# Kernel tuning notes

Hardware: AMD Instinct MI355X
Metric: run time of the kernel (lower is better)

Reference implementation:

```python
import jax, jax.numpy as jnp
import numpy as np

NUM_LEVELS = 16
LEVEL_DIM = 2
BASE_RES = 32
PER_LEVEL_SCALE = 2.0
TABLE_SIZE = 2 ** 19  # padded size of every level's table
RES = np.array([int(BASE_RES * PER_LEVEL_SCALE ** i) for i in range(NUM_LEVELS)], dtype=np.float32)
SIZES = np.minimum(RES.astype(np.float64) ** 3, TABLE_SIZE).astype(np.float32)  # true table sizes
NEAR, FAR, NUM_SAMPLES = 0.1, 1.5, 64
N_RAYS = 16384


def _xavier(key, fin, fout):
    lim = float(np.sqrt(6.0 / (fin + fout)))
    return jax.random.uniform(key, (fin, fout), jnp.float32, -lim, lim)


def setup_inputs() -> dict:
    key = jax.random.key(0)
    ks = jax.random.split(key, 12)
    rays_o = jax.random.uniform(ks[0], (N_RAYS, 3), jnp.float32, -0.5, 0.5)
    d = jax.random.normal(ks[1], (N_RAYS, 3), jnp.float32)
    rays_d = d / jnp.linalg.norm(d, axis=-1, keepdims=True)
    tables = jax.random.uniform(ks[2], (NUM_LEVELS, TABLE_SIZE, LEVEL_DIM), jnp.float32, -1e-4, 1e-4)
    return {
        'rays_o': rays_o, 'rays_d': rays_d, 'tables': tables,
        'Wg0': _xavier(ks[3], 32, 64), 'bg0': jnp.zeros((64,), jnp.float32),
        'Wg1': _xavier(ks[4], 64, 64), 'bg1': jnp.zeros((64,), jnp.float32),
        'Wd': _xavier(ks[5], 64, 16), 'bd': jnp.zeros((16,), jnp.float32),
        'Wc0': _xavier(ks[6], 24, 64), 'bc0': jnp.zeros((64,), jnp.float32),
        'Wc1': _xavier(ks[7], 64, 64), 'bc1': jnp.zeros((64,), jnp.float32),
        'Wc2': _xavier(ks[8], 64, 64), 'bc2': jnp.zeros((64,), jnp.float32),
        'Wch': _xavier(ks[9], 64, 3), 'bch': jnp.zeros((3,), jnp.float32),
    }


def _hash_encode(pts, tables):
    # pts: [N, S, 3] in roughly [-1, 1]; tables: [L, T, 2]
    res = jnp.asarray(RES)            # [L]
    sizes = jnp.asarray(SIZES)        # [L]
    scaled = (pts[..., None, :] + 1.0) / 2.0 * (res[:, None] - 1.0)     # [N,S,L,3]
    scaled = jnp.clip(scaled, 0.0, res[:, None] - 1.0)
    # torch computes the flat index in float then .long() (truncation), then clamps to table size
    idx_f = scaled[..., 0] * res * res + scaled[..., 1] * res + scaled[..., 2]  # [N,S,L]
    idx = jnp.minimum(idx_f, sizes - 1.0).astype(jnp.int32)
    feats = tables[jnp.arange(NUM_LEVELS)[None, None, :], idx]          # [N,S,L,2]
    return feats.reshape(feats.shape[:-2] + (NUM_LEVELS * LEVEL_DIM,))  # [N,S,32]


def _sh_encode(d):
    # degree-4 encoder in the source only ever builds 9 features
    x, y, z = d[..., 0], d[..., 1], d[..., 2]
    return jnp.stack([jnp.full_like(x, 0.5), x, y, z,
                      x * y, x * z, y * z, x * x - y * y, 3.0 * z * z - 1.0], axis=-1)  # [N,9]


def reference(rays_o, rays_d, tables, Wg0, bg0, Wg1, bg1, Wd, bd,
              Wc0, bc0, Wc1, bc1, Wc2, bc2, Wch, bch):
    n = rays_o.shape[0]
    # --- stratified-free (eval mode) sampling along rays ---
    t = jnp.linspace(0.0, 1.0, NUM_SAMPLES, dtype=jnp.float32)
    z_vals = jnp.broadcast_to(NEAR + (FAR - NEAR) * t, (n, NUM_SAMPLES))           # [N,S]
    pts = rays_o[:, None, :] + rays_d[:, None, :] * z_vals[..., None]              # [N,S,3]
    # --- LoDAwareNeRF forward ---
    feats = _hash_encode(pts, tables)                                              # [N,S,32]
    h = jax.nn.relu(feats @ Wg0 + bg0)
    h = jax.nn.relu(h @ Wg1 + bg1)
    geo = h @ Wd + bd                                                              # [N,S,16]
    density = jax.nn.softplus(geo[..., 0] - 1.0)                                   # [N,S]
    geo_feat = geo[..., 1:]                                                        # [N,S,15]
    dir_f = jnp.broadcast_to(_sh_encode(rays_d)[:, None, :], (n, NUM_SAMPLES, 9))  # [N,S,9]
    c = jnp.concatenate([geo_feat, dir_f], axis=-1)                                # [N,S,24]
    c = jax.nn.relu(c @ Wc0 + bc0)
    c = jax.nn.relu(c @ Wc1 + bc1)
    c = jax.nn.relu(c @ Wc2 + bc2)
    color = jax.nn.sigmoid(c @ Wch + bch)                                          # [N,S,3]
    # --- volume rendering compositing ---
    dists = z_vals[..., 1:] - z_vals[..., :-1]
    dists = jnp.concatenate([dists, jnp.full_like(dists[..., :1], 1e10)], axis=-1)
    dists = dists * jnp.linalg.norm(rays_d, axis=-1, keepdims=True)
    alpha = 1.0 - jnp.exp(-density * dists)                                        # [N,S]
    T = jnp.cumprod(1.0 - alpha + 1e-10, axis=-1)
    T = jnp.concatenate([jnp.ones_like(T[..., :1]), T[..., :-1]], axis=-1)
    weights = alpha * T                                                            # [N,S]
    rgb = jnp.sum(weights[..., None] * color, axis=-2)                             # [N,3]
    depth = jnp.sum(weights * z_vals, axis=-1)                                     # [N]
    acc = jnp.sum(weights, axis=-1)                                                # [N]
    return rgb, depth, acc, weights
```

## Files before the change

### kernel.cpp

```cpp
#include <hip/hip_runtime.h>
#include <hip/hip_bf16.h>
#include <math.h>

typedef float  f32x4 __attribute__((ext_vector_type(4)));
typedef short  s16x8 __attribute__((ext_vector_type(8)));
typedef unsigned int u32x2 __attribute__((ext_vector_type(2)));
typedef unsigned int u32x4 __attribute__((ext_vector_type(4)));

constexpr int kNRays = 16384;
constexpr int kOffDepth   = kNRays * 3;
constexpr int kOffAcc     = kOffDepth + kNRays;
constexpr int kOffWeights = kOffAcc + kNRays;

constexpr int kWg0 = 0;
constexpr int kWg1 = 2048;
constexpr int kWd  = 6144;
constexpr int kWc0 = 7168;
constexpr int kWc1 = 9216;
constexpr int kWc2 = 13312;
constexpr int kWch = 17408;
constexpr int kWsTotal = 18432;

__device__ __forceinline__ ushort f2bf(float x) {
    unsigned u = __float_as_uint(x);
    return (ushort)((u + 0x7FFFu + ((u >> 16) & 1u)) >> 16);
}
__device__ __forceinline__ unsigned pk2(float lo, float hi) {
    __hip_bfloat162 h = __float22bfloat162_rn(float2{lo, hi});
    return *reinterpret_cast<unsigned*>(&h);
}
__device__ __forceinline__ float sel4(float v0, float v1, float v2, float v3, int s) {
    float a = (s & 1) ? v1 : v0;
    float b = (s & 1) ? v3 : v2;
    return (s & 2) ? b : a;
}
__device__ __forceinline__ float wave_sum(float v) {
#pragma unroll
    for (int off = 32; off > 0; off >>= 1) v += __shfl_xor(v, off, 64);
    return v;
}

__global__ __launch_bounds__(256) void prep_weights(
    const float* __restrict__ Wg0, const float* __restrict__ Wg1,
    const float* __restrict__ Wd,  const float* __restrict__ Wc0,
    const float* __restrict__ Wc1, const float* __restrict__ Wc2,
    const float* __restrict__ Wch, const float* __restrict__ bc0,
    ushort* __restrict__ ws)
{
    const int i = blockIdx.x * 256 + threadIdx.x;
    if (i >= kWsTotal) return;
    const float* W; int FIN, FOUT, KT, base; bool dperm = false, c0bias = false;
    if (i < kWg1)      { W = Wg0; FIN = 32; FOUT = 64; KT = 1; base = kWg0; }
    else if (i < kWd)  { W = Wg1; FIN = 64; FOUT = 64; KT = 2; base = kWg1; }
    else if (i < kWc0) { W = Wd;  FIN = 64; FOUT = 16; KT = 2; base = kWd; dperm = true; }
    else if (i < kWc1) { W = Wc0; FIN = 24; FOUT = 64; KT = 1; base = kWc0; c0bias = true; }
    else if (i < kWc2) { W = Wc1; FIN = 64; FOUT = 64; KT = 2; base = kWc1; }
    else if (i < kWch) { W = Wc2; FIN = 64; FOUT = 64; KT = 2; base = kWc2; }
    else               { W = Wch; FIN = 64; FOUT = 3;  KT = 2; base = kWch; }
    const int r = i - base;
    const int e = r & 7, l = (r >> 3) & 63, t = r >> 9;
    const int kt = t % KT, mt = t / KT;
    const int k = kt * 32 + ((l >> 4) << 3) + e;
    int j = mt * 16 + (l & 15);
    if (dperm) j = (j == 15) ? 0 : j + 1;
    float w = 0.0f;
    if (k < FIN && j < FOUT) w = W[k * FOUT + j];
    if (c0bias && k == 24 && j < FOUT) w = bc0[j];
    ws[i] = f2bf(w);
}

template<int KT, bool HASBIAS>
__device__ __forceinline__ void layer64(ushort* __restrict__ Xw,
                                        const ushort* __restrict__ Aws,
                                        const float* __restrict__ bias,
                                        const int* rp, const int* wa,
                                        int g, int lane) {
    s16x8 B[KT][4];
#pragma unroll
    for (int kt = 0; kt < KT; ++kt)
#pragma unroll
        for (int nt = 0; nt < 4; ++nt)
            B[kt][nt] = *(const s16x8*)&Xw[rp[kt * 4 + nt]];
#pragma unroll
    for (int mt = 0; mt < 4; ++mt) {
        const s16x8 A0 = *(const s16x8*)&Aws[((mt * KT + 0) * 64 + lane) * 8];
        s16x8 A1;
        if constexpr (KT == 2) A1 = *(const s16x8*)&Aws[((mt * KT + 1) * 64 + lane) * 8];
        f32x4 b;
        if constexpr (HASBIAS) b = *(const f32x4*)(bias + mt * 16 + g * 4);
        else                   b = (f32x4){ 0.f, 0.f, 0.f, 0.f };
        f32x4 acc[4];
#pragma unroll
        for (int nt = 0; nt < 4; ++nt) {
            acc[nt] = b;
            acc[nt] = __builtin_amdgcn_mfma_f32_16x16x32_bf16(A0, B[0][nt], acc[nt], 0, 0, 0);
            if constexpr (KT == 2)
                acc[nt] = __builtin_amdgcn_mfma_f32_16x16x32_bf16(A1, B[1][nt], acc[nt], 0, 0, 0);
        }
#pragma unroll
        for (int nt = 0; nt < 4; ++nt) {
            const float x0 = fmaxf(acc[nt].x, 0.f), x1 = fmaxf(acc[nt].y, 0.f);
            const float x2 = fmaxf(acc[nt].z, 0.f), x3 = fmaxf(acc[nt].w, 0.f);
            *(u32x2*)&Xw[wa[mt * 4 + nt]] = (u32x2){ pk2(x0, x1), pk2(x2, x3) };
        }
    }
}

__device__ __forceinline__ void layer16(const ushort* __restrict__ Xw,
                                        const ushort* __restrict__ Aws,
                                        const int* rp, int lane, f32x4 acc[4]) {
    const s16x8 A0 = *(const s16x8*)&Aws[(0 * 64 + lane) * 8];
    const s16x8 A1 = *(const s16x8*)&Aws[(1 * 64 + lane) * 8];
#pragma unroll
    for (int nt = 0; nt < 4; ++nt) {
        const s16x8 B0 = *(const s16x8*)&Xw[rp[0 * 4 + nt]];
        acc[nt] = __builtin_amdgcn_mfma_f32_16x16x32_bf16(A0, B0, acc[nt], 0, 0, 0);
        const s16x8 B1 = *(const s16x8*)&Xw[rp[1 * 4 + nt]];
        acc[nt] = __builtin_amdgcn_mfma_f32_16x16x32_bf16(A1, B1, acc[nt], 0, 0, 0);
    }
}

__global__ __launch_bounds__(256, 4) void nerf_mfma_kernel(
    const float* __restrict__ rays_o, const float* __restrict__ rays_d,
    const float* __restrict__ tables, const ushort* __restrict__ ws,
    const float* __restrict__ bg0, const float* __restrict__ bg1,
    const float* __restrict__ bd,  const float* __restrict__ bc1,
    const float* __restrict__ bc2, const float* __restrict__ bch,
    float* __restrict__ out)
{
    __shared__ __align__(16) ushort Xs[4 * 4096];
    const int tid  = threadIdx.x;
    const int wid  = tid >> 6;
    const int lane = tid & 63;
    const int c16  = lane & 15;
    const int g    = lane >> 4;
    const int ray  = blockIdx.x * 4 + wid;
    ushort* Xw = Xs + wid * 4096;

    const float ox = rays_o[ray * 3 + 0], oy = rays_o[ray * 3 + 1], oz = rays_o[ray * 3 + 2];
    const float dx = rays_d[ray * 3 + 0], dy = rays_d[ray * 3 + 1], dz = rays_d[ray * 3 + 2];

    const float step = 1.0f / 63.0f;
    const float z  = 0.1f + 1.4f * ((float)lane * step);
    const float zn = 0.1f + 1.4f * ((float)(lane + 1) * step);

    int rp[8], wa[16];
#pragma unroll
    for (int kt = 0; kt < 2; ++kt)
#pragma unroll
        for (int nt = 0; nt < 4; ++nt)
            rp[kt * 4 + nt] = (nt * 16 + c16) * 64 + 8 * ((kt * 4 + g) ^ (c16 & 7));
#pragma unroll
    for (int mt = 0; mt < 4; ++mt)
#pragma unroll
        for (int nt = 0; nt < 4; ++nt)
            wa[mt * 4 + nt] = (nt * 16 + c16) * 64
                            + 8 * ((2 * mt + (g >> 1)) ^ (c16 & 7)) + 4 * (g & 1);

    const float2* __restrict__ tb = (const float2*)tables;
    const float tc = (float)c16 * step;
    s16x8 B0f[4];
#pragma unroll
    for (int nt = 0; nt < 4; ++nt) {
        const float ts = tc + (float)nt * (16.0f / 63.0f);
        const float zs = fmaf(1.4f, ts, 0.1f);
        const float px = fmaf(dx, zs, ox), py = fmaf(dy, zs, oy), pz = fmaf(dz, zs, oz);
        u32x4 val;
#pragma unroll
        for (int j = 0; j < 4; ++j) {
            const int lv = g * 4 + j;
            const float res = (float)(32 << lv);
            const float rm1 = res - 1.0f;
            const float h = 0.5f * rm1;
            const float sx = __builtin_amdgcn_fmed3f(fmaf(px, h, h), 0.f, rm1);
            const float sy = __builtin_amdgcn_fmed3f(fmaf(py, h, h), 0.f, rm1);
            const float sz = __builtin_amdgcn_fmed3f(fmaf(pz, h, h), 0.f, rm1);
            const float idxf = fmaf(sx, res * res, fmaf(sy, res, sz));
            const float szm1 = (lv == 0) ? 32767.f : (lv == 1) ? 262143.f : 524287.f;
            const unsigned idx = (unsigned)(int)fminf(idxf, szm1);
            const float2 f2 = tb[((unsigned)lv << 19) + idx];
            val[j] = pk2(f2.x, f2.y);
        }
        B0f[nt] = *(const s16x8*)&val;
    }

#pragma unroll
    for (int mt = 0; mt < 4; ++mt) {
        const s16x8 A0 = *(const s16x8*)&ws[kWg0 + (mt * 64 + lane) * 8];
        const f32x4 b = *(const f32x4*)(bg0 + mt * 16 + g * 4);
        f32x4 acc[4];
#pragma unroll
        for (int nt = 0; nt < 4; ++nt) {
            acc[nt] = b;
            acc[nt] = __builtin_amdgcn_mfma_f32_16x16x32_bf16(A0, B0f[nt], acc[nt], 0, 0, 0);
        }
#pragma unroll
        for (int nt = 0; nt < 4; ++nt) {
            const float x0 = fmaxf(acc[nt].x, 0.f), x1 = fmaxf(acc[nt].y, 0.f);
            const float x2 = fmaxf(acc[nt].z, 0.f), x3 = fmaxf(acc[nt].w, 0.f);
            *(u32x2*)&Xw[wa[mt * 4 + nt]] = (u32x2){ pk2(x0, x1), pk2(x2, x3) };
        }
    }

    layer64<2, true>(Xw, ws + kWg1, bg1, rp, wa, g, lane);

    f32x4 accd[4];
    {
        const float db0 = bd[g * 4 + 1];
        const float db1 = bd[g * 4 + 2];
        const float db2 = bd[g * 4 + 3];
        const int i3 = (g == 3) ? 0 : g * 4 + 4;
        const float db3 = bd[i3];
        const f32x4 b = { db0, db1, db2, db3 };
#pragma unroll
        for (int nt = 0; nt < 4; ++nt) accd[nt] = b;
    }
    layer16(Xw, ws + kWd, rp, lane, accd);
    const float lgit = sel4(__shfl(accd[0].w, 48 + c16, 64),
                            __shfl(accd[1].w, 48 + c16, 64),
                            __shfl(accd[2].w, 48 + c16, 64),
                            __shfl(accd[3].w, 48 + c16, 64), g);
#pragma unroll
    for (int nt = 0; nt < 4; ++nt)
        *(u32x2*)&Xw[wa[nt]] = (u32x2){ pk2(accd[nt].x, accd[nt].y),
                                        pk2(accd[nt].z, accd[nt].w) };
    Xw[lane * 64 + 8 * (1 ^ (lane & 7)) + 7] = 0x3F00;
    {
        u32x4 w = { pk2(dx, dy), pk2(dz, dx * dy), pk2(dx * dz, dy * dz),
                    pk2(dx * dx - dy * dy, 3.f * dz * dz - 1.f) };
        *(u32x4*)&Xw[lane * 64 + 8 * (2 ^ (lane & 7))] = w;
    }
    {
        u32x4 w = { 0x00003F80u, 0u, 0u, 0u };
        *(u32x4*)&Xw[lane * 64 + 8 * (3 ^ (lane & 7))] = w;
    }

    layer64<1, false>(Xw, ws + kWc0, nullptr, rp, wa, g, lane);
    layer64<2, true >(Xw, ws + kWc1, bc1,     rp, wa, g, lane);
    layer64<2, true >(Xw, ws + kWc2, bc2,     rp, wa, g, lane);

    f32x4 accc[4];
    {
        const float cb0 = bch[0], cb1 = bch[1], cb2 = bch[2];
        const f32x4 b = (g == 0) ? (f32x4){ cb0, cb1, cb2, 0.f } : (f32x4){ 0.f, 0.f, 0.f, 0.f };
#pragma unroll
        for (int nt = 0; nt < 4; ++nt) accc[nt] = b;
    }
    layer16(Xw, ws + kWch, rp, lane, accc);
    const float lr = sel4(__shfl(accc[0].x, c16, 64), __shfl(accc[1].x, c16, 64),
                          __shfl(accc[2].x, c16, 64), __shfl(accc[3].x, c16, 64), g);
    const float lgr = sel4(__shfl(accc[0].y, c16, 64), __shfl(accc[1].y, c16, 64),
                           __shfl(accc[2].y, c16, 64), __shfl(accc[3].y, c16, 64), g);
    const float lb = sel4(__shfl(accc[0].z, c16, 64), __shfl(accc[1].z, c16, 64),
                          __shfl(accc[2].z, c16, 64), __shfl(accc[3].z, c16, 64), g);

    const float cr = 1.f / (1.f + expf(-lr));
    const float cg = 1.f / (1.f + expf(-lgr));
    const float cb = 1.f / (1.f + expf(-lb));
    const float gx = lgit - 1.0f;
    const float density = fmaxf(gx, 0.f) + log1pf(expf(-fabsf(gx)));

    const float dnorm = sqrtf(dx * dx + dy * dy + dz * dz);
    float dist = (lane < 63) ? (zn - z) : 1e10f;
    dist *= dnorm;
    const float alpha = 1.0f - expf(-density * dist);
    float f = 1.0f - alpha + 1e-10f;
#pragma unroll
    for (int off = 1; off < 64; off <<= 1) {
        const float gg = __shfl_up(f, off, 64);
        if (lane >= off) f *= gg;
    }
    float T = __shfl_up(f, 1, 64);
    if (lane == 0) T = 1.0f;
    const float w = alpha * T;

    out[kOffWeights + ray * 64 + lane] = w;
    const float sr = wave_sum(w * cr);
    const float sg = wave_sum(w * cg);
    const float sb = wave_sum(w * cb);
    const float sd = wave_sum(w * z);
    const float sa = wave_sum(w);
    if (lane == 0) {
        out[ray * 3 + 0] = sr;
        out[ray * 3 + 1] = sg;
        out[ray * 3 + 2] = sb;
        out[kOffDepth + ray] = sd;
        out[kOffAcc + ray]   = sa;
    }
}

extern "C" void kernel_launch(void* const* d_in, const int* in_sizes, int n_in,
                              void* d_out, int out_size, void* d_ws, size_t ws_size,
                              hipStream_t stream) {
    const float* rays_o = (const float*)d_in[0];
    const float* rays_d = (const float*)d_in[1];
    const float* tables = (const float*)d_in[2];
    const float* Wg0 = (const float*)d_in[3];
    const float* bg0 = (const float*)d_in[4];
    const float* Wg1 = (const float*)d_in[5];
    const float* bg1 = (const float*)d_in[6];
    const float* Wd  = (const float*)d_in[7];
    const float* bd  = (const float*)d_in[8];
    const float* Wc0 = (const float*)d_in[9];
    const float* bc0 = (const float*)d_in[10];
    const float* Wc1 = (const float*)d_in[11];
    const float* bc1 = (const float*)d_in[12];
    const float* Wc2 = (const float*)d_in[13];
    const float* bc2 = (const float*)d_in[14];
    const float* Wch = (const float*)d_in[15];
    const float* bch = (const float*)d_in[16];
    float* out = (float*)d_out;
    ushort* wsp = (ushort*)d_ws;

    prep_weights<<<dim3((kWsTotal + 255) / 256), dim3(256), 0, stream>>>(
        Wg0, Wg1, Wd, Wc0, Wc1, Wc2, Wch, bc0, wsp);

    nerf_mfma_kernel<<<dim3(kNRays / 4), dim3(256), 0, stream>>>(
        rays_o, rays_d, tables, wsp,
        bg0, bg1, bd, bc1, bc2, bch, out);
}
```

Measured before the change: 78.86 us.

## Keep MLP activations in registers using 32x32 MFMA and permlane32 swaps

Replaces the 16x16x32 MFMA layers that round-trip activations through LDS with 32x32x16 MFMA layers whose outputs are rearranged into the next layer's B operand via permlane32_swap, removing shared memory entirely. The weight prep kernel is changed to the new A-fragment layout and also stages the density and color-head biases. This is meant to remove LDS writes and reads and the swizzle address math between layers. In exchange it raises register pressure, and launch bounds drop to 3 waves per block-occupancy hint.

```diff
diff --git a/kernel.cpp b/kernel.cpp
--- a/kernel.cpp
+++ b/kernel.cpp
@@ -2,9 +2,9 @@
 #include <hip/hip_bf16.h>
 #include <math.h>
 
-typedef float  f32x4 __attribute__((ext_vector_type(4)));
-typedef short  s16x8 __attribute__((ext_vector_type(8)));
-typedef unsigned int u32x2 __attribute__((ext_vector_type(2)));
+typedef float  f32x4  __attribute__((ext_vector_type(4)));
+typedef float  f32x16 __attribute__((ext_vector_type(16)));
+typedef short  s16x8  __attribute__((ext_vector_type(8)));
 typedef unsigned int u32x4 __attribute__((ext_vector_type(4)));
 
 constexpr int kNRays = 16384;
@@ -12,27 +12,23 @@
 constexpr int kOffAcc     = kOffDepth + kNRays;
 constexpr int kOffWeights = kOffAcc + kNRays;
 
-constexpr int kWg0 = 0;
-constexpr int kWg1 = 2048;
-constexpr int kWd  = 6144;
-constexpr int kWc0 = 7168;
-constexpr int kWc1 = 9216;
-constexpr int kWc2 = 13312;
-constexpr int kWch = 17408;
-constexpr int kWsTotal = 18432;
+constexpr int kAg0 = 0;
+constexpr int kAg1 = 2048;
+constexpr int kAd  = 6144;
+constexpr int kAc0 = 8192;
+constexpr int kAc1 = 10240;
+constexpr int kAc2 = 14336;
+constexpr int kAch = 18432;
+constexpr int kFb  = 20480;
+constexpr int kPrepTotal = 20480 + 64;
 
 __device__ __forceinline__ ushort f2bf(float x) {
     unsigned u = __float_as_uint(x);
     return (ushort)((u + 0x7FFFu + ((u >> 16) & 1u)) >> 16);
 }
 __device__ __forceinline__ unsigned pk2(float lo, float hi) {
-    __hip_bfloat162 h = __float22bfloat162_rn(float2{lo, hi});
-    return *reinterpret_cast<unsigned*>(&h);
-}
-__device__ __forceinline__ float sel4(float v0, float v1, float v2, float v3, int s) {
-    float a = (s & 1) ? v1 : v0;
-    float b = (s & 1) ? v3 : v2;
-    return (s & 2) ? b : a;
+    __hip_bfloat162 hh = __float22bfloat162_rn(float2{lo, hi});
+    return *reinterpret_cast<unsigned*>(&hh);
 }
 __device__ __forceinline__ float wave_sum(float v) {
 #pragma unroll
@@ -45,97 +41,103 @@
     const float* __restrict__ Wd,  const float* __restrict__ Wc0,
     const float* __restrict__ Wc1, const float* __restrict__ Wc2,
     const float* __restrict__ Wch, const float* __restrict__ bc0,
+    const float* __restrict__ bd,  const float* __restrict__ bch,
     ushort* __restrict__ ws)
 {
     const int i = blockIdx.x * 256 + threadIdx.x;
-    if (i >= kWsTotal) return;
-    const float* W; int FIN, FOUT, KT, base; bool dperm = false, c0bias = false;
-    if (i < kWg1)      { W = Wg0; FIN = 32; FOUT = 64; KT = 1; base = kWg0; }
-    else if (i < kWd)  { W = Wg1; FIN = 64; FOUT = 64; KT = 2; base = kWg1; }
-    else if (i < kWc0) { W = Wd;  FIN = 64; FOUT = 16; KT = 2; base = kWd; dperm = true; }
-    else if (i < kWc1) { W = Wc0; FIN = 24; FOUT = 64; KT = 1; base = kWc0; c0bias = true; }
-    else if (i < kWc2) { W = Wc1; FIN = 64; FOUT = 64; KT = 2; base = kWc1; }
-    else if (i < kWch) { W = Wc2; FIN = 64; FOUT = 64; KT = 2; base = kWc2; }
-    else               { W = Wch; FIN = 64; FOUT = 3;  KT = 2; base = kWch; }
-    const int r = i - base;
-    const int e = r & 7, l = (r >> 3) & 63, t = r >> 9;
-    const int kt = t % KT, mt = t / KT;
-    const int k = kt * 32 + ((l >> 4) << 3) + e;
-    int j = mt * 16 + (l & 15);
-    if (dperm) j = (j == 15) ? 0 : j + 1;
-    float w = 0.0f;
-    if (k < FIN && j < FOUT) w = W[k * FOUT + j];
-    if (c0bias && k == 24 && j < FOUT) w = bc0[j];
-    ws[i] = f2bf(w);
-}
-
-template<int KT, bool HASBIAS>
-__device__ __forceinline__ void layer64(ushort* __restrict__ Xw,
+    if (i >= kPrepTotal) return;
+    if (i < kFb) {
+        const float* W; int KS, base, mode = 0;
+        if (i < kAg1)      { W = Wg0; KS = 2; base = kAg0; }
+        else if (i < kAd)  { W = Wg1; KS = 4; base = kAg1; }
+        else if (i < kAc0) { W = Wd;  KS = 4; base = kAd;  mode = 1; }
+        else if (i < kAc1) { W = Wc0; KS = 2; base = kAc0; mode = 2; }
+        else if (i < kAc2) { W = Wc1; KS = 4; base = kAc1; }
+        else if (i < kAch) { W = Wc2; KS = 4; base = kAc2; }
+        else               { W = Wch; KS = 4; base = kAch; mode = 3; }
+        const int r = i - base;
+        const int e = r & 7, l = (r >> 3) & 63, f = r >> 9;
+        const int ks = f % KS, mt = f / KS;
+        const int m = mt * 32 + (l & 31);
+        const int k = ks * 16 + (l >> 5) * 8 + e;
+        float w = 0.f;
+        if (mode == 0)      w = W[k * 64 + m];
+        else if (mode == 1) w = (m < 15) ? W[k * 16 + m + 1] : (m == 15 ? W[k * 16] : 0.f);
+        else if (mode == 2) w = (k < 24) ? W[k * 64 + m] : (k == 24 ? bc0[m] : 0.f);
+        else                w = (m < 3) ? W[k * 3 + m] : 0.f;
+        ws[i] = f2bf(w);
+    } else {
+        float* fb = (float*)(ws + kFb);
+        const int t = i - kFb;
+        float v = 0.f;
+        if (t < 32) { if (t < 15) v = bd[t + 1]; else if (t == 15) v = bd[0]; }
+        else        { const int tt = t - 32; if (tt < 3) v = bch[tt]; }
+        fb[t] = v;
+    }
+}
+
+template<int KS, bool HASBIAS>
+__device__ __forceinline__ void layer32(const u32x4 (*__restrict__ Bi)[2],
                                         const ushort* __restrict__ Aws,
                                         const float* __restrict__ bias,
-                                        const int* rp, const int* wa,
-                                        int g, int lane) {
-    s16x8 B[KT][4];
-#pragma unroll
-    for (int kt = 0; kt < KT; ++kt)
-#pragma unroll
-        for (int nt = 0; nt < 4; ++nt)
-            B[kt][nt] = *(const s16x8*)&Xw[rp[kt * 4 + nt]];
-#pragma unroll
-    for (int mt = 0; mt < 4; ++mt) {
-        const s16x8 A0 = *(const s16x8*)&Aws[((mt * KT + 0) * 64 + lane) * 8];
-        s16x8 A1;
-        if constexpr (KT == 2) A1 = *(const s16x8*)&Aws[((mt * KT + 1) * 64 + lane) * 8];
-        f32x4 b;
-        if constexpr (HASBIAS) b = *(const f32x4*)(bias + mt * 16 + g * 4);
-        else                   b = (f32x4){ 0.f, 0.f, 0.f, 0.f };
-        f32x4 acc[4];
-#pragma unroll
-        for (int nt = 0; nt < 4; ++nt) {
-            acc[nt] = b;
-            acc[nt] = __builtin_amdgcn_mfma_f32_16x16x32_bf16(A0, B[0][nt], acc[nt], 0, 0, 0);
-            if constexpr (KT == 2)
-                acc[nt] = __builtin_amdgcn_mfma_f32_16x16x32_bf16(A1, B[1][nt], acc[nt], 0, 0, 0);
-        }
-#pragma unroll
-        for (int nt = 0; nt < 4; ++nt) {
-            const float x0 = fmaxf(acc[nt].x, 0.f), x1 = fmaxf(acc[nt].y, 0.f);
-            const float x2 = fmaxf(acc[nt].z, 0.f), x3 = fmaxf(acc[nt].w, 0.f);
-            *(u32x2*)&Xw[wa[mt * 4 + nt]] = (u32x2){ pk2(x0, x1), pk2(x2, x3) };
-        }
-    }
-}
-
-__device__ __forceinline__ void layer16(const ushort* __restrict__ Xw,
-                                        const ushort* __restrict__ Aws,
-                                        const int* rp, int lane, f32x4 acc[4]) {
-    const s16x8 A0 = *(const s16x8*)&Aws[(0 * 64 + lane) * 8];
-    const s16x8 A1 = *(const s16x8*)&Aws[(1 * 64 + lane) * 8];
-#pragma unroll
-    for (int nt = 0; nt < 4; ++nt) {
-        const s16x8 B0 = *(const s16x8*)&Xw[rp[0 * 4 + nt]];
-        acc[nt] = __builtin_amdgcn_mfma_f32_16x16x32_bf16(A0, B0, acc[nt], 0, 0, 0);
-        const s16x8 B1 = *(const s16x8*)&Xw[rp[1 * 4 + nt]];
-        acc[nt] = __builtin_amdgcn_mfma_f32_16x16x32_bf16(A1, B1, acc[nt], 0, 0, 0);
-    }
-}
-
-__global__ __launch_bounds__(256, 4) void nerf_mfma_kernel(
+                                        int h, int lane,
+                                        u32x4 (*__restrict__ Bo)[2]) {
+#pragma unroll
+    for (int mt = 0; mt < 2; ++mt) {
+        s16x8 A[KS];
+#pragma unroll
+        for (int ks = 0; ks < KS; ++ks)
+            A[ks] = *(const s16x8*)&Aws[((mt * KS + ks) * 64 + lane) * 8];
+        f32x4 bq[4];
+#pragma unroll
+        for (int r8 = 0; r8 < 4; ++r8) {
+            if constexpr (HASBIAS)
+                bq[r8] = *(const f32x4*)(bias + mt * 32 + 4 * h + 8 * r8);
+            else
+                bq[r8] = (f32x4){0.f, 0.f, 0.f, 0.f};
+        }
+#pragma unroll
+        for (int nt = 0; nt < 2; ++nt) {
+            f32x16 acc;
+#pragma unroll
+            for (int r8 = 0; r8 < 4; ++r8) {
+                acc[4 * r8 + 0] = bq[r8].x; acc[4 * r8 + 1] = bq[r8].y;
+                acc[4 * r8 + 2] = bq[r8].z; acc[4 * r8 + 3] = bq[r8].w;
+            }
+#pragma unroll
+            for (int ks = 0; ks < KS; ++ks)
+                acc = __builtin_amdgcn_mfma_f32_32x32x16_bf16(
+                    A[ks], *(const s16x8*)&Bi[ks][nt], acc, 0, 0, 0);
+            unsigned q[4][2];
+#pragma unroll
+            for (int r8 = 0; r8 < 4; ++r8)
+#pragma unroll
+                for (int t = 0; t < 2; ++t)
+                    q[r8][t] = pk2(fmaxf(acc[4 * r8 + 2 * t], 0.f),
+                                   fmaxf(acc[4 * r8 + 2 * t + 1], 0.f));
+#pragma unroll
+            for (int kk = 0; kk < 2; ++kk) {
+                auto s0 = __builtin_amdgcn_permlane32_swap(q[2 * kk][0], q[2 * kk + 1][0], false, false);
+                auto s1 = __builtin_amdgcn_permlane32_swap(q[2 * kk][1], q[2 * kk + 1][1], false, false);
+                Bo[2 * mt + kk][nt] = (u32x4){ s0[0], s1[0], s0[1], s1[1] };
+            }
+        }
+    }
+}
+
+__global__ __launch_bounds__(256, 3) void nerf_mfma_kernel(
     const float* __restrict__ rays_o, const float* __restrict__ rays_d,
     const float* __restrict__ tables, const ushort* __restrict__ ws,
     const float* __restrict__ bg0, const float* __restrict__ bg1,
-    const float* __restrict__ bd,  const float* __restrict__ bc1,
-    const float* __restrict__ bc2, const float* __restrict__ bch,
+    const float* __restrict__ bc1, const float* __restrict__ bc2,
     float* __restrict__ out)
 {
-    __shared__ __align__(16) ushort Xs[4 * 4096];
     const int tid  = threadIdx.x;
     const int wid  = tid >> 6;
     const int lane = tid & 63;
-    const int c16  = lane & 15;
-    const int g    = lane >> 4;
+    const int c    = lane & 31;
+    const int h    = lane >> 5;
     const int ray  = blockIdx.x * 4 + wid;
-    ushort* Xw = Xs + wid * 4096;
 
     const float ox = rays_o[ray * 3 + 0], oy = rays_o[ray * 3 + 1], oz = rays_o[ray * 3 + 2];
     const float dx = rays_d[ray * 3 + 0], dy = rays_d[ray * 3 + 1], dz = rays_d[ray * 3 + 2];
@@ -144,115 +146,116 @@
     const float z  = 0.1f + 1.4f * ((float)lane * step);
     const float zn = 0.1f + 1.4f * ((float)(lane + 1) * step);
 
-    int rp[8], wa[16];
-#pragma unroll
-    for (int kt = 0; kt < 2; ++kt)
-#pragma unroll
-        for (int nt = 0; nt < 4; ++nt)
-            rp[kt * 4 + nt] = (nt * 16 + c16) * 64 + 8 * ((kt * 4 + g) ^ (c16 & 7));
-#pragma unroll
-    for (int mt = 0; mt < 4; ++mt)
-#pragma unroll
-        for (int nt = 0; nt < 4; ++nt)
-            wa[mt * 4 + nt] = (nt * 16 + c16) * 64
-                            + 8 * ((2 * mt + (g >> 1)) ^ (c16 & 7)) + 4 * (g & 1);
-
     const float2* __restrict__ tb = (const float2*)tables;
-    const float tc = (float)c16 * step;
-    s16x8 B0f[4];
-#pragma unroll
-    for (int nt = 0; nt < 4; ++nt) {
-        const float ts = tc + (float)nt * (16.0f / 63.0f);
+    u32x4 B0[2][2];
+#pragma unroll
+    for (int nt = 0; nt < 2; ++nt) {
+        const int s = nt * 32 + c;
+        const float ts = (float)s * step;
         const float zs = fmaf(1.4f, ts, 0.1f);
         const float px = fmaf(dx, zs, ox), py = fmaf(dy, zs, oy), pz = fmaf(dz, zs, oz);
-        u32x4 val;
-#pragma unroll
-        for (int j = 0; j < 4; ++j) {
-            const int lv = g * 4 + j;
-            const float res = (float)(32 << lv);
-            const float rm1 = res - 1.0f;
-            const float h = 0.5f * rm1;
-            const float sx = __builtin_amdgcn_fmed3f(fmaf(px, h, h), 0.f, rm1);
-            const float sy = __builtin_amdgcn_fmed3f(fmaf(py, h, h), 0.f, rm1);
-            const float sz = __builtin_amdgcn_fmed3f(fmaf(pz, h, h), 0.f, rm1);
-            const float idxf = fmaf(sx, res * res, fmaf(sy, res, sz));
-            const float szm1 = (lv == 0) ? 32767.f : (lv == 1) ? 262143.f : 524287.f;
-            const unsigned idx = (unsigned)(int)fminf(idxf, szm1);
-            const float2 f2 = tb[((unsigned)lv << 19) + idx];
-            val[j] = pk2(f2.x, f2.y);
-        }
-        B0f[nt] = *(const s16x8*)&val;
-    }
-
-#pragma unroll
-    for (int mt = 0; mt < 4; ++mt) {
-        const s16x8 A0 = *(const s16x8*)&ws[kWg0 + (mt * 64 + lane) * 8];
-        const f32x4 b = *(const f32x4*)(bg0 + mt * 16 + g * 4);
-        f32x4 acc[4];
-#pragma unroll
-        for (int nt = 0; nt < 4; ++nt) {
-            acc[nt] = b;
-            acc[nt] = __builtin_amdgcn_mfma_f32_16x16x32_bf16(A0, B0f[nt], acc[nt], 0, 0, 0);
-        }
-#pragma unroll
-        for (int nt = 0; nt < 4; ++nt) {
-            const float x0 = fmaxf(acc[nt].x, 0.f), x1 = fmaxf(acc[nt].y, 0.f);
-            const float x2 = fmaxf(acc[nt].z, 0.f), x3 = fmaxf(acc[nt].w, 0.f);
-            *(u32x2*)&Xw[wa[mt * 4 + nt]] = (u32x2){ pk2(x0, x1), pk2(x2, x3) };
-        }
-    }
-
-    layer64<2, true>(Xw, ws + kWg1, bg1, rp, wa, g, lane);
-
-    f32x4 accd[4];
+#pragma unroll
+        for (int ks = 0; ks < 2; ++ks) {
+            u32x4 val;
+#pragma unroll
+            for (int j = 0; j < 4; ++j) {
+                const int lv = 8 * ks + 4 * h + j;
+                const float res = (float)(32 << lv);
+                const float rm1 = res - 1.0f;
+                const float hf = 0.5f * rm1;
+                const float sx = __builtin_amdgcn_fmed3f(fmaf(px, hf, hf), 0.f, rm1);
+                const float sy = __builtin_amdgcn_fmed3f(fmaf(py, hf, hf), 0.f, rm1);
+                const float sz = __builtin_amdgcn_fmed3f(fmaf(pz, hf, hf), 0.f, rm1);
+                const float idxf = fmaf(sx, res * res, fmaf(sy, res, sz));
+                const float szm1 = (lv == 0) ? 32767.f : (lv == 1) ? 262143.f : 524287.f;
+                const unsigned idx = (unsigned)(int)fminf(idxf, szm1);
+                const float2 f2 = tb[((unsigned)lv << 19) + idx];
+                val[j] = pk2(f2.x, f2.y);
+            }
+            B0[ks][nt] = val;
+        }
+    }
+
+    u32x4 B1[4][2], B2[4][2];
+    layer32<2, true>(B0, ws + kAg0, bg0, h, lane, B1);
+    layer32<4, true>(B1, ws + kAg1, bg1, h, lane, B2);
+
+    const float* fb = (const float*)(ws + kFb);
+    u32x4 Bc0[2][2];
+    float lg0 = 0.f, lg1 = 0.f;
     {
-        const float db0 = bd[g * 4 + 1];
-        const float db1 = bd[g * 4 + 2];
-        const float db2 = bd[g * 4 + 3];
-        const int i3 = (g == 3) ? 0 : g * 4 + 4;
-        const float db3 = bd[i3];
-        const f32x4 b = { db0, db1, db2, db3 };
-#pragma unroll
-        for (int nt = 0; nt < 4; ++nt) accd[nt] = b;
-    }
-    layer16(Xw, ws + kWd, rp, lane, accd);
-    const float lgit = sel4(__shfl(accd[0].w, 48 + c16, 64),
-                            __shfl(accd[1].w, 48 + c16, 64),
-                            __shfl(accd[2].w, 48 + c16, 64),
-                            __shfl(accd[3].w, 48 + c16, 64), g);
-#pragma unroll
-    for (int nt = 0; nt < 4; ++nt)
-        *(u32x2*)&Xw[wa[nt]] = (u32x2){ pk2(accd[nt].x, accd[nt].y),
-                                        pk2(accd[nt].z, accd[nt].w) };
-    Xw[lane * 64 + 8 * (1 ^ (lane & 7)) + 7] = 0x3F00;
+        s16x8 Ad[4];
+#pragma unroll
+        for (int ks = 0; ks < 4; ++ks)
+            Ad[ks] = *(const s16x8*)&ws[kAd + (ks * 64 + lane) * 8];
+#pragma unroll
+        for (int nt = 0; nt < 2; ++nt) {
+            f32x16 acc;
+#pragma unroll
+            for (int r8 = 0; r8 < 4; ++r8) {
+                const f32x4 bq = *(const f32x4*)(fb + 4 * h + 8 * r8);
+                acc[4 * r8 + 0] = bq.x; acc[4 * r8 + 1] = bq.y;
+                acc[4 * r8 + 2] = bq.z; acc[4 * r8 + 3] = bq.w;
+            }
+#pragma unroll
+            for (int ks = 0; ks < 4; ++ks)
+                acc = __builtin_amdgcn_mfma_f32_32x32x16_bf16(
+                    Ad[ks], *(const s16x8*)&B2[ks][nt], acc, 0, 0, 0);
+            if (nt == 0) lg0 = acc[7]; else lg1 = acc[7];
+            if (h) acc[7] = 0.5f;
+            const unsigned q00 = pk2(acc[0], acc[1]), q01 = pk2(acc[2], acc[3]);
+            const unsigned q10 = pk2(acc[4], acc[5]), q11 = pk2(acc[6], acc[7]);
+            auto s0 = __builtin_amdgcn_permlane32_swap(q00, q10, false, false);
+            auto s1 = __builtin_amdgcn_permlane32_swap(q01, q11, false, false);
+            Bc0[0][nt] = (u32x4){ s0[0], s1[0], s0[1], s1[1] };
+        }
+    }
+    float lgit;
     {
-        u32x4 w = { pk2(dx, dy), pk2(dz, dx * dy), pk2(dx * dz, dy * dz),
-                    pk2(dx * dx - dy * dy, 3.f * dz * dz - 1.f) };
-        *(u32x4*)&Xw[lane * 64 + 8 * (2 ^ (lane & 7))] = w;
+        auto sl = __builtin_amdgcn_permlane32_swap(__float_as_uint(lg0), __float_as_uint(lg1), false, false);
+        lgit = __uint_as_float(sl[1]);
     }
     {
-        u32x4 w = { 0x00003F80u, 0u, 0u, 0u };
-        *(u32x4*)&Xw[lane * 64 + 8 * (3 ^ (lane & 7))] = w;
-    }
-
-    layer64<1, false>(Xw, ws + kWc0, nullptr, rp, wa, g, lane);
-    layer64<2, true >(Xw, ws + kWc1, bc1,     rp, wa, g, lane);
-    layer64<2, true >(Xw, ws + kWc2, bc2,     rp, wa, g, lane);
-
-    f32x4 accc[4];
+        u32x4 wloc;
+        if (h == 0) wloc = (u32x4){ pk2(dx, dy), pk2(dz, dx * dy), pk2(dx * dz, dy * dz),
+                                    pk2(dx * dx - dy * dy, 3.f * dz * dz - 1.f) };
+        else        wloc = (u32x4){ 0x00003F80u, 0u, 0u, 0u };
+        Bc0[1][0] = wloc; Bc0[1][1] = wloc;
+    }
+
+    u32x4 B3[4][2], B4[4][2], B5[4][2];
+    layer32<2, false>(Bc0, ws + kAc0, nullptr, h, lane, B3);
+    layer32<4, true >(B3,  ws + kAc1, bc1,     h, lane, B4);
+    layer32<4, true >(B4,  ws + kAc2, bc2,     h, lane, B5);
+
+    f32x16 acch[2];
     {
-        const float cb0 = bch[0], cb1 = bch[1], cb2 = bch[2];
-        const f32x4 b = (g == 0) ? (f32x4){ cb0, cb1, cb2, 0.f } : (f32x4){ 0.f, 0.f, 0.f, 0.f };
-#pragma unroll
-        for (int nt = 0; nt < 4; ++nt) accc[nt] = b;
-    }
-    layer16(Xw, ws + kWch, rp, lane, accc);
-    const float lr = sel4(__shfl(accc[0].x, c16, 64), __shfl(accc[1].x, c16, 64),
-                          __shfl(accc[2].x, c16, 64), __shfl(accc[3].x, c16, 64), g);
-    const float lgr = sel4(__shfl(accc[0].y, c16, 64), __shfl(accc[1].y, c16, 64),
-                           __shfl(accc[2].y, c16, 64), __shfl(accc[3].y, c16, 64), g);
-    const float lb = sel4(__shfl(accc[0].z, c16, 64), __shfl(accc[1].z, c16, 64),
-                          __shfl(accc[2].z, c16, 64), __shfl(accc[3].z, c16, 64), g);
+        s16x8 Ah[4];
+#pragma unroll
+        for (int ks = 0; ks < 4; ++ks)
+            Ah[ks] = *(const s16x8*)&ws[kAch + (ks * 64 + lane) * 8];
+#pragma unroll
+        for (int nt = 0; nt < 2; ++nt) {
+            f32x16 acc;
+#pragma unroll
+            for (int r8 = 0; r8 < 4; ++r8) {
+                const f32x4 bq = *(const f32x4*)(fb + 32 + 4 * h + 8 * r8);
+                acc[4 * r8 + 0] = bq.x; acc[4 * r8 + 1] = bq.y;
+                acc[4 * r8 + 2] = bq.z; acc[4 * r8 + 3] = bq.w;
+            }
+#pragma unroll
+            for (int ks = 0; ks < 4; ++ks)
+                acc = __builtin_amdgcn_mfma_f32_32x32x16_bf16(
+                    Ah[ks], *(const s16x8*)&B5[ks][nt], acc, 0, 0, 0);
+            acch[nt] = acc;
+        }
+    }
+    auto sw0 = __builtin_amdgcn_permlane32_swap(__float_as_uint(acch[0][0]), __float_as_uint(acch[1][0]), false, false);
+    auto sw1 = __builtin_amdgcn_permlane32_swap(__float_as_uint(acch[0][1]), __float_as_uint(acch[1][1]), false, false);
+    auto sw2 = __builtin_amdgcn_permlane32_swap(__float_as_uint(acch[0][2]), __float_as_uint(acch[1][2]), false, false);
+    const float lr  = __uint_as_float(sw0[0]);
+    const float lgr = __uint_as_float(sw1[0]);
+    const float lb  = __uint_as_float(sw2[0]);
 
     const float cr = 1.f / (1.f + expf(-lr));
     const float cg = 1.f / (1.f + expf(-lgr));
@@ -312,10 +315,10 @@
     float* out = (float*)d_out;
     ushort* wsp = (ushort*)d_ws;
 
-    prep_weights<<<dim3((kWsTotal + 255) / 256), dim3(256), 0, stream>>>(
-        Wg0, Wg1, Wd, Wc0, Wc1, Wc2, Wch, bc0, wsp);
+    prep_weights<<<dim3((kPrepTotal + 255) / 256), dim3(256), 0, stream>>>(
+        Wg0, Wg1, Wd, Wc0, Wc1, Wc2, Wch, bc0, bd, bch, wsp);
 
     nerf_mfma_kernel<<<dim3(kNRays / 4), dim3(256), 0, stream>>>(
         rays_o, rays_d, tables, wsp,
-        bg0, bg1, bd, bc1, bc2, bch, out);
-}
+        bg0, bg1, bc1, bc2, out);
+}
```

Result: slower. 85.39 us (+8.3%).

## Keep MLP activations in registers by permuting weight K-order, drop LDS staging

Applied to the files above, without the earlier changes.

Rewrites the MLP chain so each layer's MFMA output fragment is packed directly into the next layer's B operand in registers. The prep kernel permutes the weights' input-feature order so that the C layout lines up with B. This removes the shared-memory round trip, swizzled address tables and LDS stores/loads between layers. Biases for the density and color heads are prepacked into the workspace. Launch bounds drop from 4 to 3 blocks per SM, trading occupancy for the higher register pressure.

```diff
diff --git a/kernel.cpp b/kernel.cpp
--- a/kernel.cpp
+++ b/kernel.cpp
@@ -2,9 +2,8 @@
 #include <hip/hip_bf16.h>
 #include <math.h>
 
-typedef float  f32x4 __attribute__((ext_vector_type(4)));
-typedef short  s16x8 __attribute__((ext_vector_type(8)));
-typedef unsigned int u32x2 __attribute__((ext_vector_type(2)));
+typedef float  f32x4  __attribute__((ext_vector_type(4)));
+typedef short  s16x8  __attribute__((ext_vector_type(8)));
 typedef unsigned int u32x4 __attribute__((ext_vector_type(4)));
 
 constexpr int kNRays = 16384;
@@ -12,22 +11,23 @@
 constexpr int kOffAcc     = kOffDepth + kNRays;
 constexpr int kOffWeights = kOffAcc + kNRays;
 
-constexpr int kWg0 = 0;
-constexpr int kWg1 = 2048;
-constexpr int kWd  = 6144;
-constexpr int kWc0 = 7168;
-constexpr int kWc1 = 9216;
-constexpr int kWc2 = 13312;
-constexpr int kWch = 17408;
-constexpr int kWsTotal = 18432;
+constexpr int kAg0 = 0;
+constexpr int kAg1 = 2048;
+constexpr int kAd  = 6144;
+constexpr int kAc0 = 7168;
+constexpr int kAc1 = 9216;
+constexpr int kAc2 = 13312;
+constexpr int kAch = 17408;
+constexpr int kAF  = 18432;
+constexpr int kPrepTotal = kAF + 32;
 
 __device__ __forceinline__ ushort f2bf(float x) {
     unsigned u = __float_as_uint(x);
     return (ushort)((u + 0x7FFFu + ((u >> 16) & 1u)) >> 16);
 }
 __device__ __forceinline__ unsigned pk2(float lo, float hi) {
-    __hip_bfloat162 h = __float22bfloat162_rn(float2{lo, hi});
-    return *reinterpret_cast<unsigned*>(&h);
+    __hip_bfloat162 hh = __float22bfloat162_rn(float2{lo, hi});
+    return *reinterpret_cast<unsigned*>(&hh);
 }
 __device__ __forceinline__ float sel4(float v0, float v1, float v2, float v3, int s) {
     float a = (s & 1) ? v1 : v0;
@@ -44,98 +44,85 @@
     const float* __restrict__ Wg0, const float* __restrict__ Wg1,
     const float* __restrict__ Wd,  const float* __restrict__ Wc0,
     const float* __restrict__ Wc1, const float* __restrict__ Wc2,
-    const float* __restrict__ Wch, const float* __restrict__ bc0,
-    ushort* __restrict__ ws)
+    const float* __restrict__ Wch, const float* __restrict__ bd,
+    const float* __restrict__ bch, ushort* __restrict__ ws)
 {
     const int i = blockIdx.x * 256 + threadIdx.x;
-    if (i >= kWsTotal) return;
-    const float* W; int FIN, FOUT, KT, base; bool dperm = false, c0bias = false;
-    if (i < kWg1)      { W = Wg0; FIN = 32; FOUT = 64; KT = 1; base = kWg0; }
-    else if (i < kWd)  { W = Wg1; FIN = 64; FOUT = 64; KT = 2; base = kWg1; }
-    else if (i < kWc0) { W = Wd;  FIN = 64; FOUT = 16; KT = 2; base = kWd; dperm = true; }
-    else if (i < kWc1) { W = Wc0; FIN = 24; FOUT = 64; KT = 1; base = kWc0; c0bias = true; }
-    else if (i < kWc2) { W = Wc1; FIN = 64; FOUT = 64; KT = 2; base = kWc1; }
-    else if (i < kWch) { W = Wc2; FIN = 64; FOUT = 64; KT = 2; base = kWc2; }
-    else               { W = Wch; FIN = 64; FOUT = 3;  KT = 2; base = kWch; }
+    if (i >= kPrepTotal) return;
+    if (i >= kAF) {
+        float* fb = (float*)(ws + kAF);
+        const int t = i - kAF;
+        float v = 0.f;
+        if (t < 16) v = (t < 15) ? bd[t + 1] : bd[0];
+        else { const int tt = t - 16; if (tt < 3) v = bch[tt]; }
+        fb[t] = v;
+        return;
+    }
+    const float* W; int KTP, base, mode = 0;
+    if (i < kAg1)      { W = Wg0; KTP = 1; base = kAg0; }
+    else if (i < kAd)  { W = Wg1; KTP = 2; base = kAg1; }
+    else if (i < kAc0) { W = Wd;  KTP = 2; base = kAd;  mode = 1; }
+    else if (i < kAc1) { W = Wc0; KTP = 1; base = kAc0; mode = 2; }
+    else if (i < kAc2) { W = Wc1; KTP = 2; base = kAc1; }
+    else if (i < kAch) { W = Wc2; KTP = 2; base = kAc2; }
+    else               { W = Wch; KTP = 2; base = kAch; mode = 3; }
     const int r = i - base;
-    const int e = r & 7, l = (r >> 3) & 63, t = r >> 9;
-    const int kt = t % KT, mt = t / KT;
-    const int k = kt * 32 + ((l >> 4) << 3) + e;
-    int j = mt * 16 + (l & 15);
-    if (dperm) j = (j == 15) ? 0 : j + 1;
-    float w = 0.0f;
-    if (k < FIN && j < FOUT) w = W[k * FOUT + j];
-    if (c0bias && k == 24 && j < FOUT) w = bc0[j];
+    const int e = r & 7, l = (r >> 3) & 63, f = r >> 9;
+    const int kt = f % KTP, mt = f / KTP;
+    const int g = (l >> 4) & 3, c = l & 15;
+    const int fr = 32 * kt + ((e < 4) ? (4 * g + e) : (16 + 4 * g + (e - 4)));
+    const int m = 16 * mt + c;
+    float w = 0.f;
+    if (mode == 0)      w = W[fr * 64 + m];
+    else if (mode == 1) w = (m < 15) ? W[fr * 16 + m + 1] : W[fr * 16];
+    else if (mode == 2) w = (fr < 24) ? W[fr * 64 + m] : 0.f;
+    else                w = (m < 3) ? W[fr * 3 + m] : 0.f;
     ws[i] = f2bf(w);
 }
 
-template<int KT, bool HASBIAS>
-__device__ __forceinline__ void layer64(ushort* __restrict__ Xw,
-                                        const ushort* __restrict__ Aws,
-                                        const float* __restrict__ bias,
-                                        const int* rp, const int* wa,
-                                        int g, int lane) {
-    s16x8 B[KT][4];
-#pragma unroll
-    for (int kt = 0; kt < KT; ++kt)
-#pragma unroll
-        for (int nt = 0; nt < 4; ++nt)
-            B[kt][nt] = *(const s16x8*)&Xw[rp[kt * 4 + nt]];
+template<int KTP, bool RELU>
+__device__ __forceinline__ void layerX(const u32x4 (*__restrict__ Bi)[4],
+                                       const ushort* __restrict__ Aws,
+                                       const float* __restrict__ bias,
+                                       int g4, int lane, u32x4 (*__restrict__ Bo)[4]) {
 #pragma unroll
     for (int mt = 0; mt < 4; ++mt) {
-        const s16x8 A0 = *(const s16x8*)&Aws[((mt * KT + 0) * 64 + lane) * 8];
+        const s16x8 A0 = *(const s16x8*)&Aws[((mt * KTP + 0) * 64 + lane) * 8];
         s16x8 A1;
-        if constexpr (KT == 2) A1 = *(const s16x8*)&Aws[((mt * KT + 1) * 64 + lane) * 8];
-        f32x4 b;
-        if constexpr (HASBIAS) b = *(const f32x4*)(bias + mt * 16 + g * 4);
-        else                   b = (f32x4){ 0.f, 0.f, 0.f, 0.f };
-        f32x4 acc[4];
+        if constexpr (KTP == 2) A1 = *(const s16x8*)&Aws[((mt * KTP + 1) * 64 + lane) * 8];
+        const f32x4 C = *(const f32x4*)(bias + 16 * mt + g4);
 #pragma unroll
         for (int nt = 0; nt < 4; ++nt) {
-            acc[nt] = b;
-            acc[nt] = __builtin_amdgcn_mfma_f32_16x16x32_bf16(A0, B[0][nt], acc[nt], 0, 0, 0);
-            if constexpr (KT == 2)
-                acc[nt] = __builtin_amdgcn_mfma_f32_16x16x32_bf16(A1, B[1][nt], acc[nt], 0, 0, 0);
-        }
-#pragma unroll
-        for (int nt = 0; nt < 4; ++nt) {
-            const float x0 = fmaxf(acc[nt].x, 0.f), x1 = fmaxf(acc[nt].y, 0.f);
-            const float x2 = fmaxf(acc[nt].z, 0.f), x3 = fmaxf(acc[nt].w, 0.f);
-            *(u32x2*)&Xw[wa[mt * 4 + nt]] = (u32x2){ pk2(x0, x1), pk2(x2, x3) };
-        }
-    }
-}
-
-__device__ __forceinline__ void layer16(const ushort* __restrict__ Xw,
-                                        const ushort* __restrict__ Aws,
-                                        const int* rp, int lane, f32x4 acc[4]) {
-    const s16x8 A0 = *(const s16x8*)&Aws[(0 * 64 + lane) * 8];
-    const s16x8 A1 = *(const s16x8*)&Aws[(1 * 64 + lane) * 8];
-#pragma unroll
-    for (int nt = 0; nt < 4; ++nt) {
-        const s16x8 B0 = *(const s16x8*)&Xw[rp[0 * 4 + nt]];
-        acc[nt] = __builtin_amdgcn_mfma_f32_16x16x32_bf16(A0, B0, acc[nt], 0, 0, 0);
-        const s16x8 B1 = *(const s16x8*)&Xw[rp[1 * 4 + nt]];
-        acc[nt] = __builtin_amdgcn_mfma_f32_16x16x32_bf16(A1, B1, acc[nt], 0, 0, 0);
-    }
-}
-
-__global__ __launch_bounds__(256, 4) void nerf_mfma_kernel(
+            f32x4 acc = __builtin_amdgcn_mfma_f32_16x16x32_bf16(
+                A0, __builtin_bit_cast(s16x8, Bi[0][nt]), C, 0, 0, 0);
+            if constexpr (KTP == 2)
+                acc = __builtin_amdgcn_mfma_f32_16x16x32_bf16(
+                    A1, __builtin_bit_cast(s16x8, Bi[1][nt]), acc, 0, 0, 0);
+            float x0 = acc.x, x1 = acc.y, x2 = acc.z, x3 = acc.w;
+            if constexpr (RELU) {
+                x0 = fmaxf(x0, 0.f); x1 = fmaxf(x1, 0.f);
+                x2 = fmaxf(x2, 0.f); x3 = fmaxf(x3, 0.f);
+            }
+            Bo[mt >> 1][nt][2 * (mt & 1)]     = pk2(x0, x1);
+            Bo[mt >> 1][nt][2 * (mt & 1) + 1] = pk2(x2, x3);
+        }
+    }
+}
+
+__global__ __launch_bounds__(256, 3) void nerf_mfma_kernel(
     const float* __restrict__ rays_o, const float* __restrict__ rays_d,
     const float* __restrict__ tables, const ushort* __restrict__ ws,
     const float* __restrict__ bg0, const float* __restrict__ bg1,
-    const float* __restrict__ bd,  const float* __restrict__ bc1,
-    const float* __restrict__ bc2, const float* __restrict__ bch,
-    float* __restrict__ out)
+    const float* __restrict__ bc0, const float* __restrict__ bc1,
+    const float* __restrict__ bc2, float* __restrict__ out)
 {
-    __shared__ __align__(16) ushort Xs[4 * 4096];
     const int tid  = threadIdx.x;
     const int wid  = tid >> 6;
     const int lane = tid & 63;
     const int c16  = lane & 15;
     const int g    = lane >> 4;
+    const int g4   = 4 * g;
     const int ray  = blockIdx.x * 4 + wid;
-    ushort* Xw = Xs + wid * 4096;
 
     const float ox = rays_o[ray * 3 + 0], oy = rays_o[ray * 3 + 1], oz = rays_o[ray * 3 + 2];
     const float dx = rays_d[ray * 3 + 0], dy = rays_d[ray * 3 + 1], dz = rays_d[ray * 3 + 2];
@@ -144,115 +131,96 @@
     const float z  = 0.1f + 1.4f * ((float)lane * step);
     const float zn = 0.1f + 1.4f * ((float)(lane + 1) * step);
 
-    int rp[8], wa[16];
-#pragma unroll
-    for (int kt = 0; kt < 2; ++kt)
-#pragma unroll
-        for (int nt = 0; nt < 4; ++nt)
-            rp[kt * 4 + nt] = (nt * 16 + c16) * 64 + 8 * ((kt * 4 + g) ^ (c16 & 7));
-#pragma unroll
-    for (int mt = 0; mt < 4; ++mt)
-#pragma unroll
-        for (int nt = 0; nt < 4; ++nt)
-            wa[mt * 4 + nt] = (nt * 16 + c16) * 64
-                            + 8 * ((2 * mt + (g >> 1)) ^ (c16 & 7)) + 4 * (g & 1);
-
     const float2* __restrict__ tb = (const float2*)tables;
-    const float tc = (float)c16 * step;
-    s16x8 B0f[4];
+    u32x4 B0[1][4];
 #pragma unroll
     for (int nt = 0; nt < 4; ++nt) {
-        const float ts = tc + (float)nt * (16.0f / 63.0f);
+        const int s = nt * 16 + c16;
+        const float ts = (float)s * step;
         const float zs = fmaf(1.4f, ts, 0.1f);
         const float px = fmaf(dx, zs, ox), py = fmaf(dy, zs, oy), pz = fmaf(dz, zs, oz);
         u32x4 val;
 #pragma unroll
         for (int j = 0; j < 4; ++j) {
-            const int lv = g * 4 + j;
+            const int lv = (j < 2) ? (2 * g + j) : (8 + 2 * g + (j - 2));
             const float res = (float)(32 << lv);
             const float rm1 = res - 1.0f;
-            const float h = 0.5f * rm1;
-            const float sx = __builtin_amdgcn_fmed3f(fmaf(px, h, h), 0.f, rm1);
-            const float sy = __builtin_amdgcn_fmed3f(fmaf(py, h, h), 0.f, rm1);
-            const float sz = __builtin_amdgcn_fmed3f(fmaf(pz, h, h), 0.f, rm1);
+            const float hf = 0.5f * rm1;
+            const float sx = __builtin_amdgcn_fmed3f(fmaf(px, hf, hf), 0.f, rm1);
+            const float sy = __builtin_amdgcn_fmed3f(fmaf(py, hf, hf), 0.f, rm1);
+            const float sz = __builtin_amdgcn_fmed3f(fmaf(pz, hf, hf), 0.f, rm1);
             const float idxf = fmaf(sx, res * res, fmaf(sy, res, sz));
             const float szm1 = (lv == 0) ? 32767.f : (lv == 1) ? 262143.f : 524287.f;
             const unsigned idx = (unsigned)(int)fminf(idxf, szm1);
             const float2 f2 = tb[((unsigned)lv << 19) + idx];
             val[j] = pk2(f2.x, f2.y);
         }
-        B0f[nt] = *(const s16x8*)&val;
-    }
-
-#pragma unroll
-    for (int mt = 0; mt < 4; ++mt) {
-        const s16x8 A0 = *(const s16x8*)&ws[kWg0 + (mt * 64 + lane) * 8];
-        const f32x4 b = *(const f32x4*)(bg0 + mt * 16 + g * 4);
-        f32x4 acc[4];
-#pragma unroll
-        for (int nt = 0; nt < 4; ++nt) {
-            acc[nt] = b;
-            acc[nt] = __builtin_amdgcn_mfma_f32_16x16x32_bf16(A0, B0f[nt], acc[nt], 0, 0, 0);
-        }
-#pragma unroll
-        for (int nt = 0; nt < 4; ++nt) {
-            const float x0 = fmaxf(acc[nt].x, 0.f), x1 = fmaxf(acc[nt].y, 0.f);
-            const float x2 = fmaxf(acc[nt].z, 0.f), x3 = fmaxf(acc[nt].w, 0.f);
-            *(u32x2*)&Xw[wa[mt * 4 + nt]] = (u32x2){ pk2(x0, x1), pk2(x2, x3) };
-        }
-    }
-
-    layer64<2, true>(Xw, ws + kWg1, bg1, rp, wa, g, lane);
-
+        B0[0][nt] = val;
+    }
+
+    u32x4 B1[2][4], B2[2][4];
+    layerX<1, true>(B0, ws + kAg0, bg0, g4, lane, B1);
+    layerX<2, true>(B1, ws + kAg1, bg1, g4, lane, B2);
+
+    const float* fb = (const float*)(ws + kAF);
     f32x4 accd[4];
     {
-        const float db0 = bd[g * 4 + 1];
-        const float db1 = bd[g * 4 + 2];
-        const float db2 = bd[g * 4 + 3];
-        const int i3 = (g == 3) ? 0 : g * 4 + 4;
-        const float db3 = bd[i3];
-        const f32x4 b = { db0, db1, db2, db3 };
-#pragma unroll
-        for (int nt = 0; nt < 4; ++nt) accd[nt] = b;
-    }
-    layer16(Xw, ws + kWd, rp, lane, accd);
+        const s16x8 A0 = *(const s16x8*)&ws[kAd + (0 * 64 + lane) * 8];
+        const s16x8 A1 = *(const s16x8*)&ws[kAd + (1 * 64 + lane) * 8];
+        const f32x4 Cd = *(const f32x4*)(fb + g4);
+#pragma unroll
+        for (int nt = 0; nt < 4; ++nt) {
+            f32x4 a = __builtin_amdgcn_mfma_f32_16x16x32_bf16(
+                A0, __builtin_bit_cast(s16x8, B2[0][nt]), Cd, 0, 0, 0);
+            a = __builtin_amdgcn_mfma_f32_16x16x32_bf16(
+                A1, __builtin_bit_cast(s16x8, B2[1][nt]), a, 0, 0, 0);
+            accd[nt] = a;
+        }
+    }
     const float lgit = sel4(__shfl(accd[0].w, 48 + c16, 64),
                             __shfl(accd[1].w, 48 + c16, 64),
                             __shfl(accd[2].w, 48 + c16, 64),
                             __shfl(accd[3].w, 48 + c16, 64), g);
-#pragma unroll
-    for (int nt = 0; nt < 4; ++nt)
-        *(u32x2*)&Xw[wa[nt]] = (u32x2){ pk2(accd[nt].x, accd[nt].y),
-                                        pk2(accd[nt].z, accd[nt].w) };
-    Xw[lane * 64 + 8 * (1 ^ (lane & 7)) + 7] = 0x3F00;
+    const float dxy = dx * dy, dxz = dx * dz, dyz = dy * dz;
+    const float dqq = dx * dx - dy * dy, dzz = 3.f * dz * dz - 1.f;
+    const unsigned sh0 = pk2(sel4(dx, dxz, 0.f, 0.f, g), sel4(dy, dyz, 0.f, 0.f, g));
+    const unsigned sh1 = pk2(sel4(dz, dqq, 0.f, 0.f, g), sel4(dxy, dzz, 0.f, 0.f, g));
+    u32x4 Bc0[1][4];
+#pragma unroll
+    for (int nt = 0; nt < 4; ++nt) {
+        const f32x4 a = accd[nt];
+        const float a3 = (g == 3) ? 0.5f : a.w;
+        Bc0[0][nt][0] = pk2(a.x, a.y);
+        Bc0[0][nt][1] = pk2(a.z, a3);
+        Bc0[0][nt][2] = sh0;
+        Bc0[0][nt][3] = sh1;
+    }
+
+    u32x4 B3[2][4], B4[2][4], B5[2][4];
+    layerX<1, true>(Bc0, ws + kAc0, bc0, g4, lane, B3);
+    layerX<2, true>(B3,  ws + kAc1, bc1, g4, lane, B4);
+    layerX<2, true>(B4,  ws + kAc2, bc2, g4, lane, B5);
+
+    f32x4 acch[4];
     {
-        u32x4 w = { pk2(dx, dy), pk2(dz, dx * dy), pk2(dx * dz, dy * dz),
-                    pk2(dx * dx - dy * dy, 3.f * dz * dz - 1.f) };
-        *(u32x4*)&Xw[lane * 64 + 8 * (2 ^ (lane & 7))] = w;
-    }
-    {
-        u32x4 w = { 0x00003F80u, 0u, 0u, 0u };
-        *(u32x4*)&Xw[lane * 64 + 8 * (3 ^ (lane & 7))] = w;
-    }
-
-    layer64<1, false>(Xw, ws + kWc0, nullptr, rp, wa, g, lane);
-    layer64<2, true >(Xw, ws + kWc1, bc1,     rp, wa, g, lane);
-    layer64<2, true >(Xw, ws + kWc2, bc2,     rp, wa, g, lane);
-
-    f32x4 accc[4];
-    {
-        const float cb0 = bch[0], cb1 = bch[1], cb2 = bch[2];
-        const f32x4 b = (g == 0) ? (f32x4){ cb0, cb1, cb2, 0.f } : (f32x4){ 0.f, 0.f, 0.f, 0.f };
-#pragma unroll
-        for (int nt = 0; nt < 4; ++nt) accc[nt] = b;
-    }
-    layer16(Xw, ws + kWch, rp, lane, accc);
-    const float lr = sel4(__shfl(accc[0].x, c16, 64), __shfl(accc[1].x, c16, 64),
-                          __shfl(accc[2].x, c16, 64), __shfl(accc[3].x, c16, 64), g);
-    const float lgr = sel4(__shfl(accc[0].y, c16, 64), __shfl(accc[1].y, c16, 64),
-                           __shfl(accc[2].y, c16, 64), __shfl(accc[3].y, c16, 64), g);
-    const float lb = sel4(__shfl(accc[0].z, c16, 64), __shfl(accc[1].z, c16, 64),
-                          __shfl(accc[2].z, c16, 64), __shfl(accc[3].z, c16, 64), g);
+        const s16x8 A0 = *(const s16x8*)&ws[kAch + (0 * 64 + lane) * 8];
+        const s16x8 A1 = *(const s16x8*)&ws[kAch + (1 * 64 + lane) * 8];
+        const f32x4 Cc = *(const f32x4*)(fb + 16 + g4);
+#pragma unroll
+        for (int nt = 0; nt < 4; ++nt) {
+            f32x4 a = __builtin_amdgcn_mfma_f32_16x16x32_bf16(
+                A0, __builtin_bit_cast(s16x8, B5[0][nt]), Cc, 0, 0, 0);
+            a = __builtin_amdgcn_mfma_f32_16x16x32_bf16(
+                A1, __builtin_bit_cast(s16x8, B5[1][nt]), a, 0, 0, 0);
+            acch[nt] = a;
+        }
+    }
+    const float lr  = sel4(__shfl(acch[0].x, c16, 64), __shfl(acch[1].x, c16, 64),
+                           __shfl(acch[2].x, c16, 64), __shfl(acch[3].x, c16, 64), g);
+    const float lgr = sel4(__shfl(acch[0].y, c16, 64), __shfl(acch[1].y, c16, 64),
+                           __shfl(acch[2].y, c16, 64), __shfl(acch[3].y, c16, 64), g);
+    const float lb  = sel4(__shfl(acch[0].z, c16, 64), __shfl(acch[1].z, c16, 64),
+                           __shfl(acch[2].z, c16, 64), __shfl(acch[3].z, c16, 64), g);
 
     const float cr = 1.f / (1.f + expf(-lr));
     const float cg = 1.f / (1.f + expf(-lgr));
@@ -312,10 +280,10 @@
     float* out = (float*)d_out;
     ushort* wsp = (ushort*)d_ws;
 
-    prep_weights<<<dim3((kWsTotal + 255) / 256), dim3(256), 0, stream>>>(
-        Wg0, Wg1, Wd, Wc0, Wc1, Wc2, Wch, bc0, wsp);
+    prep_weights<<<dim3((kPrepTotal + 255) / 256), dim3(256), 0, stream>>>(
+        Wg0, Wg1, Wd, Wc0, Wc1, Wc2, Wch, bd, bch, wsp);
 
     nerf_mfma_kernel<<<dim3(kNRays / 4), dim3(256), 0, stream>>>(
         rays_o, rays_d, tables, wsp,
-        bg0, bg1, bd, bc1, bc2, bch, out);
-}
+        bg0, bg1, bc0, bc1, bc2, out);
+}
```

Result: slower. 84.13 us (+6.7%).
